# Performance work log

Measured on AMD Instinct MI355X. Metric: run time of the kernel, lower is better.

The kernel has to match this reference:

```python
import jax, jax.numpy as jnp
import numpy as np

B, D_IN, D_H, N_ACT, N_HEADS = 64, 512, 512, 16, 8
EPS = 1e-6


def setup_inputs() -> dict:
    key = jax.random.key(0)
    ks = jax.random.split(key, 4)
    s = lambda fan_in: 1.0 / np.sqrt(fan_in).astype(np.float32)
    return {
        "x": jax.random.normal(ks[0], (B, D_IN), jnp.float32),
        "Wh": jax.random.normal(ks[1], (D_IN, D_H), jnp.float32) * s(D_IN),
        "bh": jnp.zeros((D_H,), jnp.float32),
        "ln_scale": jnp.ones((D_H,), jnp.float32),
        "ln_bias": jnp.zeros((D_H,), jnp.float32),
        "Wz1": jax.random.normal(ks[2], (D_IN + N_ACT, N_HEADS * D_H), jnp.float32) * s(D_IN + N_ACT),
        "Wz2": jax.random.normal(ks[3], (D_IN + N_ACT, N_HEADS * D_H), jnp.float32) * s(D_IN + N_ACT),
    }


def reference(x, Wh, bh, ln_scale, ln_bias, Wz1, Wz2):
    # h = LayerNorm(relu(fc_h(x)))
    h_pre = jax.nn.relu(x @ Wh + bh)                      # (B, D_H)
    mu = jnp.mean(h_pre, axis=-1, keepdims=True)
    var = jnp.var(h_pre, axis=-1, keepdims=True)
    h = (h_pre - mu) / jnp.sqrt(var + EPS) * ln_scale + ln_bias

    # input conditioning: repeat x per action, concat one-hot action
    x_rep = jnp.repeat(x, N_ACT, axis=0)                  # (B*A, D_IN)
    onehot = jnp.tile(jnp.eye(N_ACT, dtype=jnp.float32), (x.shape[0], 1))
    xc = jnp.concatenate([x_rep, onehot], axis=-1)        # (B*A, D_IN+A)

    z1 = (xc @ Wz1).reshape(-1, N_HEADS, D_H)             # (B*A, H, D_H)
    z2 = (xc @ Wz2).reshape(-1, N_HEADS, D_H)             # (B*A, H, D_G=D_H)

    # bilinear scores over tiny contraction dim H, then row norm + tanh
    w = jnp.einsum('bhg,bhd->bgd', z2, z1)                # (B*A, D_G, D_H)
    w = (w - jnp.mean(w, axis=-1, keepdims=True)) / (jnp.std(w, axis=-1, keepdims=True) + EPS)
    w = jnp.tanh(w)

    v = jnp.repeat(h, N_ACT, axis=0)                      # (B*A, D_H)
    y_ = jnp.einsum('bgd,bd->bg', w, v)                   # (B*A, D_G)

    # goodness 'msq'
    logits = jnp.mean(jnp.square(y_), axis=1)[:, None]    # (B*A, 1)
    q = logits.reshape(-1, N_ACT)                         # (B, A)
    return h, q, y_
```

## Files before the change

kernel.cpp:

```cpp
#include <hip/hip_runtime.h>
#include <math.h>

#define EPS 1e-6f

typedef _Float16 half8 __attribute__((ext_vector_type(8)));
typedef _Float16 half2v __attribute__((ext_vector_type(2)));
typedef __fp16  fp16x2r __attribute__((ext_vector_type(2)));
typedef float f32x16 __attribute__((ext_vector_type(16)));

__device__ __forceinline__ half2v cvt_pk(float a, float b) {
    fp16x2r v = __builtin_amdgcn_cvt_pkrtz(a, b);
    return __builtin_bit_cast(half2v, v);
}

__device__ __forceinline__ float fdot2f(half2v a, half2v b, float c) {
#if __has_builtin(__builtin_amdgcn_fdot2)
    return __builtin_amdgcn_fdot2(__builtin_bit_cast(fp16x2r, a),
                                  __builtin_bit_cast(fp16x2r, b), c, false);
#else
    return fmaf((float)a[0], (float)b[0], fmaf((float)a[1], (float)b[1], c));
#endif
}

__device__ __forceinline__ float tile_finish(const f32x16& D, uint4 va, uint4 vb,
                                             float yg) {
    const half2v CLO = {(_Float16)-2.5f, (_Float16)-2.5f};
    const half2v CHI = {(_Float16) 2.5f, (_Float16) 2.5f};
    const half2v C0  = {(_Float16)0.98335470f, (_Float16)0.98335470f};
    const half2v C1  = {(_Float16)-0.24780080f, (_Float16)-0.24780080f};
    const half2v C2  = {(_Float16)0.04040730f, (_Float16)0.04040730f};
    const half2v C3  = {(_Float16)-0.00252110f, (_Float16)-0.00252110f};
#define PAIR(jj, word) {                                          \
        half2v tt = cvt_pk(D[2*jj], D[2*jj+1]);                   \
        tt = __builtin_elementwise_max(tt, CLO);                  \
        tt = __builtin_elementwise_min(tt, CHI);                  \
        half2v u  = tt * tt;                                      \
        half2v pp = C3 * u + C2;                                  \
        pp = pp * u + C1;                                         \
        pp = pp * u + C0;                                         \
        half2v wt = tt * pp;                                      \
        yg = fdot2f(wt, __builtin_bit_cast(half2v, word), yg); }
    PAIR(0, va.x) PAIR(1, va.y) PAIR(2, va.z) PAIR(3, va.w)
    PAIR(4, vb.x) PAIR(5, vb.y) PAIR(6, vb.z) PAIR(7, vb.w)
#undef PAIR
    return yg;
}

__global__ __launch_bounds__(256) void k_xh(
    const float* __restrict__ x, _Float16* __restrict__ xh,
    float* __restrict__ zbuf) {
    const int tid = blockIdx.x * 256 + threadIdx.x;
    const int i = tid * 8;
    float4 a = *(const float4*)(x + i);
    float4 b = *(const float4*)(x + i + 4);
    half8 o;
    o[0] = (_Float16)a.x; o[1] = (_Float16)a.y; o[2] = (_Float16)a.z; o[3] = (_Float16)a.w;
    o[4] = (_Float16)b.x; o[5] = (_Float16)b.y; o[6] = (_Float16)b.z; o[7] = (_Float16)b.w;
    *(half8*)(xh + i) = o;

    const float4 z = {0.f, 0.f, 0.f, 0.f};
#pragma unroll 2
    for (int j = tid * 4; j < 557056; j += 4096 * 4)
        *(float4*)(zbuf + j) = z;
}

__global__ __launch_bounds__(256) void k_gemm(
    const _Float16* __restrict__ xh, const float* __restrict__ Wh,
    const float* __restrict__ Wz1, const float* __restrict__ Wz2,
    float* __restrict__ hpre, float* __restrict__ xz1,
    float* __restrict__ xz2) {
    const int s  = blockIdx.x;
    const int k0 = blockIdx.y * 256;
    const int t  = threadIdx.x;
    const int l  = t & 63, w = t >> 6;
    const int hi = l >> 5, l31 = l & 31;
    const int cbase = s * 128;

    const float* __restrict__ W;
    float* __restrict__ out;
    int ncols, ocol;
    if (s < 4)       { W = Wh;  out = hpre; ncols = 512;  ocol = cbase; }
    else if (s < 36) { W = Wz1; out = xz1;  ncols = 4096; ocol = cbase - 512; }
    else             { W = Wz2; out = xz2;  ncols = 4096; ocol = cbase - 4608; }

    const int col = ocol + 32 * w + l31;

    const f32x16 CZ = {0.f, 0.f, 0.f, 0.f, 0.f, 0.f, 0.f, 0.f,
                       0.f, 0.f, 0.f, 0.f, 0.f, 0.f, 0.f, 0.f};
    f32x16 acc0 = CZ;
    f32x16 acc1 = CZ;

    const _Float16* __restrict__ a0p = xh + l31 * 512 + 8 * hi + k0;
    const _Float16* __restrict__ a1p = a0p + 32 * 512;
    const float* __restrict__    wp  = W + (size_t)(k0 + 8 * hi) * ncols + col;

#pragma unroll 2
    for (int kk = 0; kk < 256; kk += 16) {
        half8 a0 = *(const half8*)(a0p + kk);
        half8 a1 = *(const half8*)(a1p + kk);
        const float* wk = wp + (size_t)kk * ncols;
        half8 bf;
#pragma unroll
        for (int j = 0; j < 8; ++j)
            bf[j] = (_Float16)wk[(size_t)j * ncols];
        acc0 = __builtin_amdgcn_mfma_f32_32x32x16_f16(a0, bf, acc0, 0, 0, 0);
        acc1 = __builtin_amdgcn_mfma_f32_32x32x16_f16(a1, bf, acc1, 0, 0, 0);
    }
#pragma unroll
    for (int i = 0; i < 16; ++i) {
        const int m = (i & 3) + 8 * (i >> 2) + 4 * hi;
        atomicAdd(out + (size_t)m * ncols + col,        acc0[i]);
        atomicAdd(out + (size_t)(m + 32) * ncols + col, acc1[i]);
    }
}

__global__ __launch_bounds__(256) void k_mid(
    const float* __restrict__ hpre, const float* __restrict__ bh,
    const float* __restrict__ ls, const float* __restrict__ lb,
    const float* __restrict__ xz1, const float* __restrict__ xz2,
    const float* __restrict__ Wz1, const float* __restrict__ Wz2,
    float* __restrict__ hout,
    _Float16* __restrict__ z1h, _Float16* __restrict__ z2h,
    _Float16* __restrict__ z2bh) {
    const int t  = threadIdx.x;
    const int l  = t & 63, wv = t >> 6;

    __shared__ float red[44 * 4];
    __shared__ float Ssum[44];

    if (blockIdx.x < 64) {
        const int b = blockIdx.x;
        float h0 = fmaxf(hpre[b * 512 + t]       + bh[t],       0.f);
        float h1 = fmaxf(hpre[b * 512 + t + 256] + bh[t + 256], 0.f);
        float s = h0 + h1, ss = h0 * h0 + h1 * h1;
#pragma unroll
        for (int m = 1; m < 64; m <<= 1) {
            s  += __shfl_xor(s, m);
            ss += __shfl_xor(ss, m);
        }
        if (l == 0) { red[wv] = s; red[4 + wv] = ss; }
        __syncthreads();
        s  = red[0] + red[1] + red[2] + red[3];
        ss = red[4] + red[5] + red[6] + red[7];
        float mean = s * (1.0f / 512.0f);
        float var  = ss * (1.0f / 512.0f) - mean * mean;
        float rstd = rsqrtf(var + EPS);
        hout[b * 512 + t]       = (h0 - mean) * rstd * ls[t]       + lb[t];
        hout[b * 512 + t + 256] = (h1 - mean) * rstd * ls[t + 256] + lb[t + 256];
        return;
    }

    const int r  = blockIdx.x - 64;
    const int br = r >> 4, a = r & 15;

    const float* __restrict__ x1  = xz1 + br * 4096;
    const float* __restrict__ x2  = xz2 + br * 4096;
    const float* __restrict__ w1r = Wz1 + (512 + a) * 4096;
    const float* __restrict__ w2r = Wz2 + (512 + a) * 4096;

    float pm[8], pg[36];
#pragma unroll
    for (int i = 0; i < 8; ++i) pm[i] = 0.f;
#pragma unroll
    for (int i = 0; i < 36; ++i) pg[i] = 0.f;

    half8 h2keep[2];
#pragma unroll
    for (int p = 0; p < 2; ++p) {
        const int d = t + p * 256;
        half8 h1, h2;
#pragma unroll
        for (int h = 0; h < 8; ++h) {
            float z1v = x1[h * 512 + d] + w1r[h * 512 + d];
            float z2v = x2[h * 512 + d] + w2r[h * 512 + d];
            h1[h] = (_Float16)z1v;
            h2[h] = (_Float16)z2v;
        }
        *(half8*)(z1h + ((size_t)r * 512 + d) * 8) = h1;
        h2keep[p] = h2;
        float zr[8];
#pragma unroll
        for (int h = 0; h < 8; ++h) zr[h] = (float)h1[h];
#pragma unroll
        for (int h = 0; h < 8; ++h) pm[h] += zr[h];
        int id = 0;
#pragma unroll
        for (int h = 0; h < 8; ++h)
#pragma unroll
            for (int h2_ = h; h2_ < 8; ++h2_) { pg[id] += zr[h] * zr[h2_]; ++id; }
    }

#pragma unroll
    for (int m = 1; m < 64; m <<= 1) {
#pragma unroll
        for (int i = 0; i < 8; ++i)  pm[i] += __shfl_xor(pm[i], m);
#pragma unroll
        for (int i = 0; i < 36; ++i) pg[i] += __shfl_xor(pg[i], m);
    }
    if (l == 0) {
#pragma unroll
        for (int i = 0; i < 8; ++i)  red[i * 4 + wv]       = pm[i];
#pragma unroll
        for (int i = 0; i < 36; ++i) red[(8 + i) * 4 + wv] = pg[i];
    }
    __syncthreads();
    if (t < 44) Ssum[t] = red[t * 4 + 0] + red[t * 4 + 1] + red[t * 4 + 2] + red[t * 4 + 3];
    __syncthreads();

#pragma unroll
    for (int p = 0; p < 2; ++p) {
        const int g = t + p * 256;
        float zv[8];
#pragma unroll
        for (int h = 0; h < 8; ++h) zv[h] = (float)h2keep[p][h];
        float mean = 0.f;
#pragma unroll
        for (int h = 0; h < 8; ++h) mean = fmaf(zv[h], Ssum[h], mean);
        mean *= (1.0f / 512.0f);
        float e2 = 0.f;
        int id = 0;
#pragma unroll
        for (int h = 0; h < 8; ++h)
#pragma unroll
            for (int h2_ = h; h2_ < 8; ++h2_) {
                float p2 = zv[h] * zv[h2_] * Ssum[8 + id];
                e2 += (h2_ == h) ? p2 : 2.0f * p2;
                ++id;
            }
        e2 *= (1.0f / 512.0f);
        float var  = e2 - mean * mean;
        float sd   = sqrtf(fmaxf(var, 0.f));
        float rstd = 1.0f / (sd + EPS);
        z2bh[r * 512 + g] = (_Float16)(-mean * rstd);
        half8 hs;
#pragma unroll
        for (int h = 0; h < 8; ++h) hs[h] = (_Float16)(zv[h] * rstd);
        *(half8*)(z2h + ((size_t)r * 512 + g) * 8) = hs;
    }
}

__global__ __launch_bounds__(256, 4) void k_main(
    const _Float16* __restrict__ z1h, const _Float16* __restrict__ z2h,
    const _Float16* __restrict__ z2bh, const float* __restrict__ hbuf,
    float* __restrict__ yout, float* __restrict__ qout) {
    const int r  = blockIdx.x;
    const int br = r >> 4;
    const int t  = threadIdx.x;
    const int l  = t & 63, wv = t >> 6;
    const int hi = l >> 5, l31 = l & 31;

    __shared__ __align__(16) _Float16 z1t[513 * 8];
    __shared__ __align__(16) unsigned int vp[256];
    __shared__ float wq[4];

#pragma unroll
    for (int p = 0; p < 2; ++p) {
        const int d = t + p * 256;
        *(half8*)(z1t + d * 8) = *(const half8*)(z1h + ((size_t)r * 512 + d) * 8);
    }
    if (t == 0) {
        half8 one = {};
        one[0] = (_Float16)1.0f;
        *(half8*)(z1t + 512 * 8) = one;
    }
    {
        const float* __restrict__ vrow = hbuf + br * 512;
        const int mm = t >> 4, h2 = (t >> 3) & 1, j = t & 7;
        const int d0 = mm * 32 + 2 * (j & 1) + 8 * (j >> 1) + 4 * h2;
        vp[t] = __builtin_bit_cast(unsigned int, cvt_pk(vrow[d0], vrow[d0 + 1]));
    }
    __syncthreads();

    const size_t gb = (size_t)r * 512 + wv * 128 + l31;
    half8 Bf0, Bf1, Bf2, Bf3;
    if (hi) {
        half8 z = {};
        Bf0 = z; Bf0[0] = z2bh[gb];
        Bf1 = z; Bf1[0] = z2bh[gb + 32];
        Bf2 = z; Bf2[0] = z2bh[gb + 64];
        Bf3 = z; Bf3[0] = z2bh[gb + 96];
    } else {
        Bf0 = *(const half8*)(z2h + gb * 8);
        Bf1 = *(const half8*)(z2h + (gb + 32) * 8);
        Bf2 = *(const half8*)(z2h + (gb + 64) * 8);
        Bf3 = *(const half8*)(z2h + (gb + 96) * 8);
    }

    const f32x16 CZ = {0.f, 0.f, 0.f, 0.f, 0.f, 0.f, 0.f, 0.f,
                       0.f, 0.f, 0.f, 0.f, 0.f, 0.f, 0.f, 0.f};
    float yg0 = 0.f, yg1 = 0.f, yg2 = 0.f, yg3 = 0.f;
#pragma unroll 2
    for (int m = 0; m < 16; ++m) {
        const int arow = hi ? 512 : (m * 32 + l31);
        const half8 Aa = *(const half8*)(z1t + arow * 8);
        const uint4 va = *(const uint4*)(vp + (m * 2 + hi) * 8);
        const uint4 vb = *(const uint4*)(vp + (m * 2 + hi) * 8 + 4);
        f32x16 D0 = __builtin_amdgcn_mfma_f32_32x32x16_f16(Aa, Bf0, CZ, 0, 0, 0);
        yg0 = tile_finish(D0, va, vb, yg0);
        f32x16 D1 = __builtin_amdgcn_mfma_f32_32x32x16_f16(Aa, Bf1, CZ, 0, 0, 0);
        yg1 = tile_finish(D1, va, vb, yg1);
        f32x16 D2 = __builtin_amdgcn_mfma_f32_32x32x16_f16(Aa, Bf2, CZ, 0, 0, 0);
        yg2 = tile_finish(D2, va, vb, yg2);
        f32x16 D3 = __builtin_amdgcn_mfma_f32_32x32x16_f16(Aa, Bf3, CZ, 0, 0, 0);
        yg3 = tile_finish(D3, va, vb, yg3);
    }

    yg0 += __shfl_xor(yg0, 32);
    yg1 += __shfl_xor(yg1, 32);
    yg2 += __shfl_xor(yg2, 32);
    yg3 += __shfl_xor(yg3, 32);

    const int gy = r * 512 + wv * 128 + l31;
    if (!hi) {
        yout[gy]      = yg0;
        yout[gy + 32] = yg1;
        yout[gy + 64] = yg2;
        yout[gy + 96] = yg3;
    }
    float qacc = hi ? 0.f : (yg0 * yg0 + yg1 * yg1 + yg2 * yg2 + yg3 * yg3);
#pragma unroll
    for (int m = 1; m < 64; m <<= 1) qacc += __shfl_xor(qacc, m);
    if (l == 0) wq[wv] = qacc;
    __syncthreads();
    if (t == 0) qout[r] = (wq[0] + wq[1] + wq[2] + wq[3]) * (1.0f / 512.0f);
}

extern "C" void kernel_launch(void* const* d_in, const int* in_sizes, int n_in,
                              void* d_out, int out_size, void* d_ws, size_t ws_size,
                              hipStream_t stream) {
    const float* x   = (const float*)d_in[0];
    const float* Wh  = (const float*)d_in[1];
    const float* bh  = (const float*)d_in[2];
    const float* ls  = (const float*)d_in[3];
    const float* lb  = (const float*)d_in[4];
    const float* Wz1 = (const float*)d_in[5];
    const float* Wz2 = (const float*)d_in[6];

    float* out  = (float*)d_out;
    float* hout = out;
    float* qout = out + 32768;
    float* yout = out + 33792;

    char* ws = (char*)d_ws;
    float*     xz1  = (float*)(ws);
    float*     xz2  = (float*)(ws + (1u << 20));
    float*     hpre = (float*)(ws + (2u << 20));
    _Float16*  xh   = (_Float16*)(ws + (2u << 20) + 135168);
    _Float16*  z2bh = (_Float16*)(ws + (2u << 20) + 200704);
    _Float16*  z1h  = (_Float16*)(ws + (4u << 20));
    _Float16*  z2h  = z1h + (size_t)1024 * 512 * 8;

    k_xh  <<<16, 256, 0, stream>>>(x, xh, (float*)ws);
    k_gemm<<<dim3(68, 2), 256, 0, stream>>>(xh, Wh, Wz1, Wz2, hpre, xz1, xz2);
    k_mid <<<1088, 256, 0, stream>>>(hpre, bh, ls, lb, xz1, xz2, Wz1, Wz2,
                                     hout, z1h, z2h, z2bh);
    k_main<<<1024, 256, 0, stream>>>(z1h, z2h, z2bh, hout, yout, qout);
}
```

Before: 80.36 us.

## Split k_main rows across two blocks along g with atomic q accumulation

Each k_main block now handles half of the 512 output columns of a row, so the launch grows from 1024 to 2048 blocks and each wave runs two MFMA tiles per step instead of four. The q logit is accumulated with atomicAdd from the two halves, and qout is zeroed in k_xh beforehand. This raises parallelism and lowers register pressure per wave. In exchange, the z1 tile and the v vector are loaded into shared memory twice as often, and the q result now depends on atomics.

```diff
diff --git a/kernel.cpp b/kernel.cpp
--- a/kernel.cpp
+++ b/kernel.cpp
@@ -48,7 +48,7 @@
 
 __global__ __launch_bounds__(256) void k_xh(
     const float* __restrict__ x, _Float16* __restrict__ xh,
-    float* __restrict__ zbuf) {
+    float* __restrict__ zbuf, float* __restrict__ qout) {
     const int tid = blockIdx.x * 256 + threadIdx.x;
     const int i = tid * 8;
     float4 a = *(const float4*)(x + i);
@@ -62,6 +62,7 @@
 #pragma unroll 2
     for (int j = tid * 4; j < 557056; j += 4096 * 4)
         *(float4*)(zbuf + j) = z;
+    if (tid < 256) *(float4*)(qout + tid * 4) = z;
 }
 
 __global__ __launch_bounds__(256) void k_gemm(
@@ -243,7 +244,8 @@
     const _Float16* __restrict__ z1h, const _Float16* __restrict__ z2h,
     const _Float16* __restrict__ z2bh, const float* __restrict__ hbuf,
     float* __restrict__ yout, float* __restrict__ qout) {
-    const int r  = blockIdx.x;
+    const int bx = blockIdx.x;
+    const int r  = bx >> 1, gh = bx & 1;
     const int br = r >> 4;
     const int t  = threadIdx.x;
     const int l  = t & 63, wv = t >> 6;
@@ -271,24 +273,20 @@
     }
     __syncthreads();
 
-    const size_t gb = (size_t)r * 512 + wv * 128 + l31;
-    half8 Bf0, Bf1, Bf2, Bf3;
+    const size_t gb = (size_t)r * 512 + gh * 256 + wv * 64 + l31;
+    half8 Bf0, Bf1;
     if (hi) {
         half8 z = {};
         Bf0 = z; Bf0[0] = z2bh[gb];
         Bf1 = z; Bf1[0] = z2bh[gb + 32];
-        Bf2 = z; Bf2[0] = z2bh[gb + 64];
-        Bf3 = z; Bf3[0] = z2bh[gb + 96];
     } else {
         Bf0 = *(const half8*)(z2h + gb * 8);
         Bf1 = *(const half8*)(z2h + (gb + 32) * 8);
-        Bf2 = *(const half8*)(z2h + (gb + 64) * 8);
-        Bf3 = *(const half8*)(z2h + (gb + 96) * 8);
     }
 
     const f32x16 CZ = {0.f, 0.f, 0.f, 0.f, 0.f, 0.f, 0.f, 0.f,
                        0.f, 0.f, 0.f, 0.f, 0.f, 0.f, 0.f, 0.f};
-    float yg0 = 0.f, yg1 = 0.f, yg2 = 0.f, yg3 = 0.f;
+    float yg0 = 0.f, yg1 = 0.f;
 #pragma unroll 2
     for (int m = 0; m < 16; ++m) {
         const int arow = hi ? 512 : (m * 32 + l31);
@@ -299,30 +297,22 @@
         yg0 = tile_finish(D0, va, vb, yg0);
         f32x16 D1 = __builtin_amdgcn_mfma_f32_32x32x16_f16(Aa, Bf1, CZ, 0, 0, 0);
         yg1 = tile_finish(D1, va, vb, yg1);
-        f32x16 D2 = __builtin_amdgcn_mfma_f32_32x32x16_f16(Aa, Bf2, CZ, 0, 0, 0);
-        yg2 = tile_finish(D2, va, vb, yg2);
-        f32x16 D3 = __builtin_amdgcn_mfma_f32_32x32x16_f16(Aa, Bf3, CZ, 0, 0, 0);
-        yg3 = tile_finish(D3, va, vb, yg3);
     }
 
     yg0 += __shfl_xor(yg0, 32);
     yg1 += __shfl_xor(yg1, 32);
-    yg2 += __shfl_xor(yg2, 32);
-    yg3 += __shfl_xor(yg3, 32);
-
-    const int gy = r * 512 + wv * 128 + l31;
+
+    const int gy = r * 512 + gh * 256 + wv * 64 + l31;
     if (!hi) {
         yout[gy]      = yg0;
         yout[gy + 32] = yg1;
-        yout[gy + 64] = yg2;
-        yout[gy + 96] = yg3;
-    }
-    float qacc = hi ? 0.f : (yg0 * yg0 + yg1 * yg1 + yg2 * yg2 + yg3 * yg3);
+    }
+    float qacc = hi ? 0.f : (yg0 * yg0 + yg1 * yg1);
 #pragma unroll
     for (int m = 1; m < 64; m <<= 1) qacc += __shfl_xor(qacc, m);
     if (l == 0) wq[wv] = qacc;
     __syncthreads();
-    if (t == 0) qout[r] = (wq[0] + wq[1] + wq[2] + wq[3]) * (1.0f / 512.0f);
+    if (t == 0) atomicAdd(qout + r, (wq[0] + wq[1] + wq[2] + wq[3]) * (1.0f / 512.0f));
 }
 
 extern "C" void kernel_launch(void* const* d_in, const int* in_sizes, int n_in,
@@ -350,9 +340,9 @@
     _Float16*  z1h  = (_Float16*)(ws + (4u << 20));
     _Float16*  z2h  = z1h + (size_t)1024 * 512 * 8;
 
-    k_xh  <<<16, 256, 0, stream>>>(x, xh, (float*)ws);
+    k_xh  <<<16, 256, 0, stream>>>(x, xh, (float*)ws, qout);
     k_gemm<<<dim3(68, 2), 256, 0, stream>>>(xh, Wh, Wz1, Wz2, hpre, xz1, xz2);
     k_mid <<<1088, 256, 0, stream>>>(hpre, bh, ls, lb, xz1, xz2, Wz1, Wz2,
                                      hout, z1h, z2h, z2bh);
-    k_main<<<1024, 256, 0, stream>>>(z1h, z2h, z2bh, hout, yout, qout);
-}
+    k_main<<<2048, 256, 0, stream>>>(z1h, z2h, z2bh, hout, yout, qout);
+}
```

Measured after the change: 80.14 us. About the same (-0.3%).

## Fuse z-prep into main bilinear kernel via LDS and split GEMM grid finer

Applied to the files above, without the earlier changes.

Merges the per-row z1/z2 normalization kernel with the main MFMA/tanh/reduction kernel, so the fp16 z1, z2 and bias tiles stay in shared memory instead of being written to and re-read from global workspace. LayerNorm moves into its own small kernel. The input GEMM gets a finer grid: 64-column, 32-row tiles with 128 threads, giving 544 blocks instead of 136. The conversion kernel launches more blocks to zero the accumulators. This removes roughly 16MB of intermediate global traffic and one launch, but adds a kernel and doubles the redundant W reads, since each weight tile is now loaded by two row blocks. LDS per block also grows, which may cut occupancy.

```diff
diff --git a/kernel.cpp b/kernel.cpp
--- a/kernel.cpp
+++ b/kernel.cpp
@@ -50,37 +50,38 @@
     const float* __restrict__ x, _Float16* __restrict__ xh,
     float* __restrict__ zbuf) {
     const int tid = blockIdx.x * 256 + threadIdx.x;
-    const int i = tid * 8;
-    float4 a = *(const float4*)(x + i);
-    float4 b = *(const float4*)(x + i + 4);
-    half8 o;
-    o[0] = (_Float16)a.x; o[1] = (_Float16)a.y; o[2] = (_Float16)a.z; o[3] = (_Float16)a.w;
-    o[4] = (_Float16)b.x; o[5] = (_Float16)b.y; o[6] = (_Float16)b.z; o[7] = (_Float16)b.w;
-    *(half8*)(xh + i) = o;
-
+    if (tid < 4096) {
+        const int i = tid * 8;
+        float4 a = *(const float4*)(x + i);
+        float4 b = *(const float4*)(x + i + 4);
+        half8 o;
+        o[0] = (_Float16)a.x; o[1] = (_Float16)a.y; o[2] = (_Float16)a.z; o[3] = (_Float16)a.w;
+        o[4] = (_Float16)b.x; o[5] = (_Float16)b.y; o[6] = (_Float16)b.z; o[7] = (_Float16)b.w;
+        *(half8*)(xh + i) = o;
+    }
     const float4 z = {0.f, 0.f, 0.f, 0.f};
-#pragma unroll 2
-    for (int j = tid * 4; j < 557056; j += 4096 * 4)
+    for (int j = tid * 4; j < 557056; j += 16384 * 4)
         *(float4*)(zbuf + j) = z;
 }
 
-__global__ __launch_bounds__(256) void k_gemm(
+__global__ __launch_bounds__(128) void k_gemm(
     const _Float16* __restrict__ xh, const float* __restrict__ Wh,
     const float* __restrict__ Wz1, const float* __restrict__ Wz2,
     float* __restrict__ hpre, float* __restrict__ xz1,
     float* __restrict__ xz2) {
     const int s  = blockIdx.x;
     const int k0 = blockIdx.y * 256;
+    const int r0 = blockIdx.z * 32;
     const int t  = threadIdx.x;
     const int l  = t & 63, w = t >> 6;
     const int hi = l >> 5, l31 = l & 31;
-    const int cbase = s * 128;
+    const int cbase = s * 64;
 
     const float* __restrict__ W;
     float* __restrict__ out;
     int ncols, ocol;
-    if (s < 4)       { W = Wh;  out = hpre; ncols = 512;  ocol = cbase; }
-    else if (s < 36) { W = Wz1; out = xz1;  ncols = 4096; ocol = cbase - 512; }
+    if (s < 8)       { W = Wh;  out = hpre; ncols = 512;  ocol = cbase; }
+    else if (s < 72) { W = Wz1; out = xz1;  ncols = 4096; ocol = cbase - 512; }
     else             { W = Wz2; out = xz2;  ncols = 4096; ocol = cbase - 4608; }
 
     const int col = ocol + 32 * w + l31;
@@ -88,70 +89,85 @@
     const f32x16 CZ = {0.f, 0.f, 0.f, 0.f, 0.f, 0.f, 0.f, 0.f,
                        0.f, 0.f, 0.f, 0.f, 0.f, 0.f, 0.f, 0.f};
     f32x16 acc0 = CZ;
-    f32x16 acc1 = CZ;
-
-    const _Float16* __restrict__ a0p = xh + l31 * 512 + 8 * hi + k0;
-    const _Float16* __restrict__ a1p = a0p + 32 * 512;
+
+    const _Float16* __restrict__ a0p = xh + (r0 + l31) * 512 + 8 * hi + k0;
     const float* __restrict__    wp  = W + (size_t)(k0 + 8 * hi) * ncols + col;
 
 #pragma unroll 2
     for (int kk = 0; kk < 256; kk += 16) {
         half8 a0 = *(const half8*)(a0p + kk);
-        half8 a1 = *(const half8*)(a1p + kk);
         const float* wk = wp + (size_t)kk * ncols;
         half8 bf;
 #pragma unroll
         for (int j = 0; j < 8; ++j)
             bf[j] = (_Float16)wk[(size_t)j * ncols];
         acc0 = __builtin_amdgcn_mfma_f32_32x32x16_f16(a0, bf, acc0, 0, 0, 0);
-        acc1 = __builtin_amdgcn_mfma_f32_32x32x16_f16(a1, bf, acc1, 0, 0, 0);
     }
 #pragma unroll
     for (int i = 0; i < 16; ++i) {
         const int m = (i & 3) + 8 * (i >> 2) + 4 * hi;
-        atomicAdd(out + (size_t)m * ncols + col,        acc0[i]);
-        atomicAdd(out + (size_t)(m + 32) * ncols + col, acc1[i]);
-    }
-}
-
-__global__ __launch_bounds__(256) void k_mid(
+        atomicAdd(out + (size_t)(r0 + m) * ncols + col, acc0[i]);
+    }
+}
+
+__global__ __launch_bounds__(256) void k_ln(
     const float* __restrict__ hpre, const float* __restrict__ bh,
     const float* __restrict__ ls, const float* __restrict__ lb,
+    float* __restrict__ hout) {
+    const int t = threadIdx.x;
+    const int l = t & 63, wv = t >> 6;
+    __shared__ float red[8];
+
+    const int b = blockIdx.x;
+    float h0 = fmaxf(hpre[b * 512 + t]       + bh[t],       0.f);
+    float h1 = fmaxf(hpre[b * 512 + t + 256] + bh[t + 256], 0.f);
+    float s = h0 + h1, ss = h0 * h0 + h1 * h1;
+#pragma unroll
+    for (int m = 1; m < 64; m <<= 1) {
+        s  += __shfl_xor(s, m);
+        ss += __shfl_xor(ss, m);
+    }
+    if (l == 0) { red[wv] = s; red[4 + wv] = ss; }
+    __syncthreads();
+    s  = red[0] + red[1] + red[2] + red[3];
+    ss = red[4] + red[5] + red[6] + red[7];
+    float mean = s * (1.0f / 512.0f);
+    float var  = ss * (1.0f / 512.0f) - mean * mean;
+    float rstd = rsqrtf(var + EPS);
+    hout[b * 512 + t]       = (h0 - mean) * rstd * ls[t]       + lb[t];
+    hout[b * 512 + t + 256] = (h1 - mean) * rstd * ls[t + 256] + lb[t + 256];
+}
+
+__global__ __launch_bounds__(256) void k_fused(
     const float* __restrict__ xz1, const float* __restrict__ xz2,
     const float* __restrict__ Wz1, const float* __restrict__ Wz2,
-    float* __restrict__ hout,
-    _Float16* __restrict__ z1h, _Float16* __restrict__ z2h,
-    _Float16* __restrict__ z2bh) {
+    const float* __restrict__ hbuf,
+    float* __restrict__ yout, float* __restrict__ qout) {
+    const int r  = blockIdx.x;
+    const int br = r >> 4, a = r & 15;
     const int t  = threadIdx.x;
     const int l  = t & 63, wv = t >> 6;
-
+    const int hi = l >> 5, l31 = l & 31;
+
+    __shared__ __align__(16) _Float16 z1t[513 * 8];
+    __shared__ __align__(16) _Float16 z2t[512 * 8];
+    __shared__ _Float16 bsh[512];
+    __shared__ __align__(16) unsigned int vp[256];
     __shared__ float red[44 * 4];
     __shared__ float Ssum[44];
-
-    if (blockIdx.x < 64) {
-        const int b = blockIdx.x;
-        float h0 = fmaxf(hpre[b * 512 + t]       + bh[t],       0.f);
-        float h1 = fmaxf(hpre[b * 512 + t + 256] + bh[t + 256], 0.f);
-        float s = h0 + h1, ss = h0 * h0 + h1 * h1;
-#pragma unroll
-        for (int m = 1; m < 64; m <<= 1) {
-            s  += __shfl_xor(s, m);
-            ss += __shfl_xor(ss, m);
-        }
-        if (l == 0) { red[wv] = s; red[4 + wv] = ss; }
-        __syncthreads();
-        s  = red[0] + red[1] + red[2] + red[3];
-        ss = red[4] + red[5] + red[6] + red[7];
-        float mean = s * (1.0f / 512.0f);
-        float var  = ss * (1.0f / 512.0f) - mean * mean;
-        float rstd = rsqrtf(var + EPS);
-        hout[b * 512 + t]       = (h0 - mean) * rstd * ls[t]       + lb[t];
-        hout[b * 512 + t + 256] = (h1 - mean) * rstd * ls[t + 256] + lb[t + 256];
-        return;
-    }
-
-    const int r  = blockIdx.x - 64;
-    const int br = r >> 4, a = r & 15;
+    __shared__ float wq[4];
+
+    {
+        const float* __restrict__ vrow = hbuf + br * 512;
+        const int mm = t >> 4, h2 = (t >> 3) & 1, j = t & 7;
+        const int d0 = mm * 32 + 2 * (j & 1) + 8 * (j >> 1) + 4 * h2;
+        vp[t] = __builtin_bit_cast(unsigned int, cvt_pk(vrow[d0], vrow[d0 + 1]));
+    }
+    if (t == 0) {
+        half8 one = {};
+        one[0] = (_Float16)1.0f;
+        *(half8*)(z1t + 512 * 8) = one;
+    }
 
     const float* __restrict__ x1  = xz1 + br * 4096;
     const float* __restrict__ x2  = xz2 + br * 4096;
@@ -176,7 +192,7 @@
             h1[h] = (_Float16)z1v;
             h2[h] = (_Float16)z2v;
         }
-        *(half8*)(z1h + ((size_t)r * 512 + d) * 8) = h1;
+        *(half8*)(z1t + d * 8) = h1;
         h2keep[p] = h2;
         float zr[8];
 #pragma unroll
@@ -231,59 +247,27 @@
         float var  = e2 - mean * mean;
         float sd   = sqrtf(fmaxf(var, 0.f));
         float rstd = 1.0f / (sd + EPS);
-        z2bh[r * 512 + g] = (_Float16)(-mean * rstd);
+        bsh[g] = (_Float16)(-mean * rstd);
         half8 hs;
 #pragma unroll
         for (int h = 0; h < 8; ++h) hs[h] = (_Float16)(zv[h] * rstd);
-        *(half8*)(z2h + ((size_t)r * 512 + g) * 8) = hs;
-    }
-}
-
-__global__ __launch_bounds__(256, 4) void k_main(
-    const _Float16* __restrict__ z1h, const _Float16* __restrict__ z2h,
-    const _Float16* __restrict__ z2bh, const float* __restrict__ hbuf,
-    float* __restrict__ yout, float* __restrict__ qout) {
-    const int r  = blockIdx.x;
-    const int br = r >> 4;
-    const int t  = threadIdx.x;
-    const int l  = t & 63, wv = t >> 6;
-    const int hi = l >> 5, l31 = l & 31;
-
-    __shared__ __align__(16) _Float16 z1t[513 * 8];
-    __shared__ __align__(16) unsigned int vp[256];
-    __shared__ float wq[4];
-
-#pragma unroll
-    for (int p = 0; p < 2; ++p) {
-        const int d = t + p * 256;
-        *(half8*)(z1t + d * 8) = *(const half8*)(z1h + ((size_t)r * 512 + d) * 8);
-    }
-    if (t == 0) {
-        half8 one = {};
-        one[0] = (_Float16)1.0f;
-        *(half8*)(z1t + 512 * 8) = one;
-    }
-    {
-        const float* __restrict__ vrow = hbuf + br * 512;
-        const int mm = t >> 4, h2 = (t >> 3) & 1, j = t & 7;
-        const int d0 = mm * 32 + 2 * (j & 1) + 8 * (j >> 1) + 4 * h2;
-        vp[t] = __builtin_bit_cast(unsigned int, cvt_pk(vrow[d0], vrow[d0 + 1]));
-    }
-    __syncthreads();
-
-    const size_t gb = (size_t)r * 512 + wv * 128 + l31;
+        *(half8*)(z2t + g * 8) = hs;
+    }
+    __syncthreads();
+
+    const int gbl = wv * 128 + l31;
     half8 Bf0, Bf1, Bf2, Bf3;
     if (hi) {
         half8 z = {};
-        Bf0 = z; Bf0[0] = z2bh[gb];
-        Bf1 = z; Bf1[0] = z2bh[gb + 32];
-        Bf2 = z; Bf2[0] = z2bh[gb + 64];
-        Bf3 = z; Bf3[0] = z2bh[gb + 96];
+        Bf0 = z; Bf0[0] = bsh[gbl];
+        Bf1 = z; Bf1[0] = bsh[gbl + 32];
+        Bf2 = z; Bf2[0] = bsh[gbl + 64];
+        Bf3 = z; Bf3[0] = bsh[gbl + 96];
     } else {
-        Bf0 = *(const half8*)(z2h + gb * 8);
-        Bf1 = *(const half8*)(z2h + (gb + 32) * 8);
-        Bf2 = *(const half8*)(z2h + (gb + 64) * 8);
-        Bf3 = *(const half8*)(z2h + (gb + 96) * 8);
+        Bf0 = *(const half8*)(z2t + gbl * 8);
+        Bf1 = *(const half8*)(z2t + (gbl + 32) * 8);
+        Bf2 = *(const half8*)(z2t + (gbl + 64) * 8);
+        Bf3 = *(const half8*)(z2t + (gbl + 96) * 8);
     }
 
     const f32x16 CZ = {0.f, 0.f, 0.f, 0.f, 0.f, 0.f, 0.f, 0.f,
@@ -346,13 +330,9 @@
     float*     xz2  = (float*)(ws + (1u << 20));
     float*     hpre = (float*)(ws + (2u << 20));
     _Float16*  xh   = (_Float16*)(ws + (2u << 20) + 135168);
-    _Float16*  z2bh = (_Float16*)(ws + (2u << 20) + 200704);
-    _Float16*  z1h  = (_Float16*)(ws + (4u << 20));
-    _Float16*  z2h  = z1h + (size_t)1024 * 512 * 8;
-
-    k_xh  <<<16, 256, 0, stream>>>(x, xh, (float*)ws);
-    k_gemm<<<dim3(68, 2), 256, 0, stream>>>(xh, Wh, Wz1, Wz2, hpre, xz1, xz2);
-    k_mid <<<1088, 256, 0, stream>>>(hpre, bh, ls, lb, xz1, xz2, Wz1, Wz2,
-                                     hout, z1h, z2h, z2bh);
-    k_main<<<1024, 256, 0, stream>>>(z1h, z2h, z2bh, hout, yout, qout);
-}
+
+    k_xh   <<<64, 256, 0, stream>>>(x, xh, (float*)ws);
+    k_gemm <<<dim3(136, 2, 2), 128, 0, stream>>>(xh, Wh, Wz1, Wz2, hpre, xz1, xz2);
+    k_ln   <<<64, 256, 0, stream>>>(hpre, bh, ls, lb, hout);
+    k_fused<<<1024, 256, 0, stream>>>(xz1, xz2, Wz1, Wz2, hout, yout, qout);
+}
```

Result: no change. 79.35 us (-1.3%).
